# Kernel tuning notes

Measured on AMD Instinct MI355X. Metric: run time of the kernel, lower is better.

Reference implementation:

```python
import jax, jax.numpy as jnp
import numpy as np

H = 20  # hidden size (hardcoded in the torch module)

def setup_inputs() -> dict:
    key = jax.random.key(0)
    ks = jax.random.split(key, 7)
    s = 0.1  # keep activations in a sane range for tanh/sigmoid
    return {
        "x":     jax.random.normal(ks[0], (8192, 512, 12), dtype=jnp.float32),
        "w_ih":  jax.random.normal(ks[1], (4 * H, 12), dtype=jnp.float32) * s,
        "w_hh":  jax.random.normal(ks[2], (4 * H, H), dtype=jnp.float32) * s,
        "b_ih":  jax.random.normal(ks[3], (4 * H,), dtype=jnp.float32) * s,
        "b_hh":  jax.random.normal(ks[4], (4 * H,), dtype=jnp.float32) * s,
        "w_out": jax.random.normal(ks[5], (10, H), dtype=jnp.float32) * s,
        "b_out": jax.random.normal(ks[6], (10,), dtype=jnp.float32) * s,
    }

def reference(x, w_ih, w_hh, b_ih, b_hh, w_out, b_out):
    # x: [B, T, I]. Single-layer LSTM (PyTorch gate order i,f,g,o), zero init state,
    # then Linear on the last hidden state.
    B, T, _ = x.shape
    # Precompute input projections for all timesteps: [T, B, 4H]
    x_proj = jnp.einsum('bti,gi->tbg', x, w_ih) + (b_ih + b_hh)

    def step(carry, xt):
        h, c = carry                      # each [B, H]
        gates = xt + h @ w_hh.T           # [B, 4H]
        i, f, g, o = jnp.split(gates, 4, axis=-1)
        i = jax.nn.sigmoid(i)
        f = jax.nn.sigmoid(f)
        g = jnp.tanh(g)
        o = jax.nn.sigmoid(o)
        c = f * c + i * g
        h = o * jnp.tanh(c)
        return (h, c), None

    h0 = jnp.zeros((B, H), dtype=x.dtype)
    c0 = jnp.zeros((B, H), dtype=x.dtype)
    (h_last, _), _ = jax.lax.scan(step, (h0, c0), x_proj)
    # out = Linear(h_T): r_out[:, -1, :] == h_n for a single-layer LSTM
    return h_last @ w_out.T + b_out
```

## Files before the change

### kernel.cpp

```cpp
#include <hip/hip_runtime.h>

typedef _Float16 f16;
typedef f16 f16x8 __attribute__((ext_vector_type(8)));
typedef float f32x4 __attribute__((ext_vector_type(4)));

#define T_STEPS 512
#define INPUT   12
#define HID     20
#define KDIM    32
#define BATCH   16
#define WPB     5
#define BLOCK   (WPB * 64)

static __device__ __forceinline__ void wave_lds_fence() {
    asm volatile("s_waitcnt lgkmcnt(0)" ::: "memory");
}
static __device__ __forceinline__ void block_barrier() {
    asm volatile("s_waitcnt lgkmcnt(0)\n\ts_barrier" ::: "memory");
}

static __device__ __forceinline__ float fast_sigmoid(float x) {
    float e = __builtin_amdgcn_exp2f(-1.4426950408889634f * x);
    return __builtin_amdgcn_rcpf(1.0f + e);
}
static __device__ __forceinline__ float fast_tanh(float x) {
    float e = __builtin_amdgcn_exp2f(2.8853900817779268f * x);
    return 1.0f - 2.0f * __builtin_amdgcn_rcpf(1.0f + e);
}

__global__ __launch_bounds__(BLOCK) void lstm_kernel(
    const float* __restrict__ x,
    const float* __restrict__ w_ih,
    const float* __restrict__ w_hh,
    const float* __restrict__ b_ih,
    const float* __restrict__ b_hh,
    const float* __restrict__ w_out,
    const float* __restrict__ b_out,
    float* __restrict__ out)
{
    __shared__ __align__(16) f16   Wc[80][KDIM];
    __shared__ __align__(16) f16   Abuf[2][BATCH][KDIM];
    __shared__ __align__(16) float wgbuf[WPB][16][16];

    const int tid  = threadIdx.x;
    const int wid  = tid >> 6;
    const int lane = tid & 63;

    for (int i = tid; i < 80 * KDIM; i += BLOCK) {
        int n = i >> 5, k = i & 31;
        int w = n >> 4, c = n & 15;
        int u = 4 * w + (c >> 2);
        int g = c & 3;
        int row = g * HID + u;
        float v = (k < INPUT) ? w_ih[row * INPUT + k] : w_hh[row * HID + (k - INPUT)];
        Wc[n][k] = (f16)v;
    }

    const int arow = lane & 15;
    const int aq   = lane >> 4;
    const int j  = lane & 3;
    const int uu = (lane >> 2) & 3;
    const int b  = 4 * aq + j;
    const int u  = 4 * wid + uu;

    float bias0 = b_ih[0 * HID + u] + b_hh[0 * HID + u];
    float bias1 = b_ih[1 * HID + u] + b_hh[1 * HID + u];
    float bias2 = b_ih[2 * HID + u] + b_hh[2 * HID + u];
    float bias3 = b_ih[3 * HID + u] + b_hh[3 * HID + u];

    Abuf[0][b][INPUT + u] = (f16)0.f;

    const bool xload = (wid < 4) && (lane < 48);
    const int  xb    = 4 * wid + lane / 12;
    const int  xi    = lane % 12;
    const float* xptr = x + (size_t)(blockIdx.x * BATCH + xb) * (T_STEPS * INPUT) + xi;

    float xv = 0.f;
    if (xload) {
        Abuf[0][xb][xi] = (f16)xptr[0];
        xv = xptr[INPUT];
    }
    __syncthreads();

    f16x8 bfrag = *(const f16x8*)&Wc[16 * wid + arow][aq * 8];

    float cc = 0.f;
    int p = 0;

#pragma unroll 1
    for (int t = 0; t < T_STEPS; ++t) {
        f16x8 afrag = *(const f16x8*)&Abuf[p][arow][aq * 8];

        if (xload) Abuf[p ^ 1][xb][xi] = (f16)xv;
        int tn = t + 2; if (tn > T_STEPS - 1) tn = T_STEPS - 1;
        if (xload) xv = xptr[(size_t)tn * INPUT];

        f32x4 z = {};
        f32x4 acc = __builtin_amdgcn_mfma_f32_16x16x32_f16(afrag, bfrag, z, 0, 0, 0);

        *(f32x4*)&wgbuf[wid][arow][4 * aq] = acc;
        wave_lds_fence();

        float gi = wgbuf[wid][4 * uu + 0][b] + bias0;
        float gf = wgbuf[wid][4 * uu + 1][b] + bias1;
        float gg = wgbuf[wid][4 * uu + 2][b] + bias2;
        float go = wgbuf[wid][4 * uu + 3][b] + bias3;

        float ig = fast_sigmoid(gi), fg = fast_sigmoid(gf);
        float gt = fast_tanh(gg),    og = fast_sigmoid(go);
        cc = fg * cc + ig * gt;
        float h = og * fast_tanh(cc);

        Abuf[p ^ 1][b][INPUT + u] = (f16)h;
        block_barrier();
        p ^= 1;
    }

    if (tid < BATCH * 10) {
        int ob = tid / 10, oo = tid % 10;
        float s = b_out[oo];
#pragma unroll
        for (int u2 = 0; u2 < HID; ++u2)
            s += w_out[oo * HID + u2] * (float)Abuf[0][ob][INPUT + u2];
        out[(size_t)(blockIdx.x * BATCH + ob) * 10 + oo] = s;
    }
}

extern "C" void kernel_launch(void* const* d_in, const int* in_sizes, int n_in,
                              void* d_out, int out_size, void* d_ws, size_t ws_size,
                              hipStream_t stream) {
    const float* x     = (const float*)d_in[0];
    const float* w_ih  = (const float*)d_in[1];
    const float* w_hh  = (const float*)d_in[2];
    const float* b_ih  = (const float*)d_in[3];
    const float* b_hh  = (const float*)d_in[4];
    const float* w_out = (const float*)d_in[5];
    const float* b_out = (const float*)d_in[6];
    float* out = (float*)d_out;

    const int blocks = 8192 / BATCH;
    hipLaunchKernelGGL(lstm_kernel, dim3(blocks), dim3(BLOCK), 0, stream,
                       x, w_ih, w_hh, b_ih, b_hh, w_out, b_out, out);
}
```

Before: 468.6 us.

## Swap MFMA operands so each lane holds all four gates, skipping LDS transpose

Swaps the MFMA operand roles so the weights are the A operand and the hidden/input state the B operand. The gate rows are interleaved so that each lane's four output registers are the i,f,g,o gates of one unit and batch. This removes the per-step LDS round trip (store accumulator, fence, four scattered reads) and folds the bias into the MFMA accumulator input. The state buffer gets a padded stride of 40 to reduce bank conflicts. The x-loading threads are also redistributed across waves.

```diff
diff --git a/kernel.cpp b/kernel.cpp
--- a/kernel.cpp
+++ b/kernel.cpp
@@ -8,13 +8,11 @@
 #define INPUT   12
 #define HID     20
 #define KDIM    32
+#define BSTRIDE 40
 #define BATCH   16
 #define WPB     5
 #define BLOCK   (WPB * 64)
 
-static __device__ __forceinline__ void wave_lds_fence() {
-    asm volatile("s_waitcnt lgkmcnt(0)" ::: "memory");
-}
 static __device__ __forceinline__ void block_barrier() {
     asm volatile("s_waitcnt lgkmcnt(0)\n\ts_barrier" ::: "memory");
 }
@@ -38,80 +36,69 @@
     const float* __restrict__ b_out,
     float* __restrict__ out)
 {
-    __shared__ __align__(16) f16   Wc[80][KDIM];
-    __shared__ __align__(16) f16   Abuf[2][BATCH][KDIM];
-    __shared__ __align__(16) float wgbuf[WPB][16][16];
+    __shared__ __align__(16) f16 Wc[80][KDIM];
+    __shared__ __align__(16) f16 Bbuf[2][BATCH][BSTRIDE];
 
     const int tid  = threadIdx.x;
     const int wid  = tid >> 6;
     const int lane = tid & 63;
+    const int col  = lane & 15;
+    const int quad = lane >> 4;
 
     for (int i = tid; i < 80 * KDIM; i += BLOCK) {
         int n = i >> 5, k = i & 31;
-        int w = n >> 4, c = n & 15;
-        int u = 4 * w + (c >> 2);
-        int g = c & 3;
+        int g = n & 3;
+        int u = 4 * (n >> 4) + ((n >> 2) & 3);
         int row = g * HID + u;
         float v = (k < INPUT) ? w_ih[row * INPUT + k] : w_hh[row * HID + (k - INPUT)];
         Wc[n][k] = (f16)v;
     }
 
-    const int arow = lane & 15;
-    const int aq   = lane >> 4;
-    const int j  = lane & 3;
-    const int uu = (lane >> 2) & 3;
-    const int b  = 4 * aq + j;
-    const int u  = 4 * wid + uu;
+    const int b = col;
+    const int u = 4 * wid + quad;
 
-    float bias0 = b_ih[0 * HID + u] + b_hh[0 * HID + u];
-    float bias1 = b_ih[1 * HID + u] + b_hh[1 * HID + u];
-    float bias2 = b_ih[2 * HID + u] + b_hh[2 * HID + u];
-    float bias3 = b_ih[3 * HID + u] + b_hh[3 * HID + u];
+    f32x4 cbias;
+#pragma unroll
+    for (int g = 0; g < 4; ++g)
+        cbias[g] = b_ih[g * HID + u] + b_hh[g * HID + u];
 
-    Abuf[0][b][INPUT + u] = (f16)0.f;
+    Bbuf[0][b][INPUT + u] = (f16)0.f;
 
-    const bool xload = (wid < 4) && (lane < 48);
-    const int  xb    = 4 * wid + lane / 12;
-    const int  xi    = lane % 12;
+    const bool xload = tid < BATCH * INPUT;
+    const int  xb    = tid / INPUT;
+    const int  xi    = tid % INPUT;
     const float* xptr = x + (size_t)(blockIdx.x * BATCH + xb) * (T_STEPS * INPUT) + xi;
 
     float xv = 0.f;
     if (xload) {
-        Abuf[0][xb][xi] = (f16)xptr[0];
+        Bbuf[0][xb][xi] = (f16)xptr[0];
         xv = xptr[INPUT];
     }
     __syncthreads();
 
-    f16x8 bfrag = *(const f16x8*)&Wc[16 * wid + arow][aq * 8];
+    const f16x8 afragW = *(const f16x8*)&Wc[16 * wid + col][quad * 8];
 
     float cc = 0.f;
     int p = 0;
 
 #pragma unroll 1
     for (int t = 0; t < T_STEPS; ++t) {
-        f16x8 afrag = *(const f16x8*)&Abuf[p][arow][aq * 8];
+        f16x8 bfrag = *(const f16x8*)&Bbuf[p][col][quad * 8];
 
-        if (xload) Abuf[p ^ 1][xb][xi] = (f16)xv;
+        if (xload) Bbuf[p ^ 1][xb][xi] = (f16)xv;
         int tn = t + 2; if (tn > T_STEPS - 1) tn = T_STEPS - 1;
         if (xload) xv = xptr[(size_t)tn * INPUT];
 
-        f32x4 z = {};
-        f32x4 acc = __builtin_amdgcn_mfma_f32_16x16x32_f16(afrag, bfrag, z, 0, 0, 0);
+        f32x4 acc = __builtin_amdgcn_mfma_f32_16x16x32_f16(afragW, bfrag, cbias, 0, 0, 0);
 
-        *(f32x4*)&wgbuf[wid][arow][4 * aq] = acc;
-        wave_lds_fence();
-
-        float gi = wgbuf[wid][4 * uu + 0][b] + bias0;
-        float gf = wgbuf[wid][4 * uu + 1][b] + bias1;
-        float gg = wgbuf[wid][4 * uu + 2][b] + bias2;
-        float go = wgbuf[wid][4 * uu + 3][b] + bias3;
-
-        float ig = fast_sigmoid(gi), fg = fast_sigmoid(gf);
-        float gt = fast_tanh(gg),    og = fast_sigmoid(go);
+        float ig = fast_sigmoid(acc[0]);
+        float fg = fast_sigmoid(acc[1]);
+        float gt = fast_tanh(acc[2]);
+        float og = fast_sigmoid(acc[3]);
         cc = fg * cc + ig * gt;
         float h = og * fast_tanh(cc);
 
-        Abuf[p ^ 1][b][INPUT + u] = (f16)h;
+        Bbuf[p ^ 1][b][INPUT + u] = (f16)h;
         block_barrier();
         p ^= 1;
     }
@@ -121,7 +108,7 @@
         float s = b_out[oo];
 #pragma unroll
         for (int u2 = 0; u2 < HID; ++u2)
-            s += w_out[oo * HID + u2] * (float)Abuf[0][ob][INPUT + u2];
+            s += w_out[oo * HID + u2] * (float)Bbuf[0][ob][INPUT + u2];
         out[(size_t)(blockIdx.x * BATCH + ob) * 10 + oo] = s;
     }
 }
```

After: 428.2 us. 8.6% less time.
